# Kernel tuning notes

Hardware: AMD Instinct MI355X
Metric: run time of the kernel (lower is better)

The kernel has to match this reference:

```python
import jax, jax.numpy as jnp
import numpy as np

B, T = 4096, 2048
ETA = 10.0  # constant['eta']


def setup_inputs() -> dict:
    key = jax.random.key(0)
    k0, k1, k2 = jax.random.split(key, 3)
    return {
        "inputs": jax.random.normal(k0, (B, T, 2), dtype=jnp.float32),  # [:,:,0]=eps, [:,:,1]=hs (step size)
        "W1": jax.random.normal(k1, (2, 16), dtype=jnp.float32) * 0.5,
        "b1": jnp.zeros((16,), dtype=jnp.float32),
        "W2": jax.random.normal(k2, (16, 1), dtype=jnp.float32) * 0.5,
        "b2": jnp.zeros((1,), dtype=jnp.float32),
    }


def reference(inputs, W1, b1, W2, b2):
    # GSM recurrent cell: e = MLP([eps, gamma]); sig = de/deps; gamma' = gamma - hs/eta * de/dgamma.
    # Analytic gradient of scalar e w.r.t. x (softplus' = sigmoid):
    #   de/dx = (sigmoid(x @ W1 + b1) * W2[:, 0]) @ W1.T      # [B, 2]
    inv_eta = 1.0 / ETA
    w2 = W2[:, 0]  # [16]

    def step(gamma, inp_t):  # gamma: [B,1], inp_t: [B,2]
        eps = inp_t[:, 0:1]
        hs = inp_t[:, 1:2]
        x = jnp.concatenate([eps, gamma], axis=1)            # [B,2]
        z1 = x @ W1 + b1                                     # [B,16]
        de_dx = (jax.nn.sigmoid(z1) * w2) @ W1.T             # [B,2]
        sig = de_dx[:, 0:1]                                  # de/deps
        gamma_n = gamma - hs * inv_eta * de_dx[:, 1:2]       # de/dgamma update
        return gamma_n, sig

    gamma0 = jnp.zeros((inputs.shape[0], 1), dtype=inputs.dtype)
    _, sig_seq = jax.lax.scan(step, gamma0, jnp.swapaxes(inputs, 0, 1))  # sig_seq: [T,B,1]
    return jnp.swapaxes(sig_seq, 0, 1)  # [B,T,1]
```

## Files before the change

kernel.cpp:

```cpp
#include <hip/hip_runtime.h>

#define B_ROWS 4096
#define T_LEN  2048
#define TB     16
#define NBLK   (T_LEN / TB)

template<int CTRL>
__device__ __forceinline__ float dpp_add(float x) {
  int y = __builtin_amdgcn_update_dpp(0, __builtin_bit_cast(int, x),
                                      CTRL, 0xf, 0xf, true);
  return x + __builtin_bit_cast(float, y);
}

__device__ __forceinline__ float allreduce16(float x) {
  x = dpp_add<0xB1>(x);
  x = dpp_add<0x4E>(x);
  x = dpp_add<0x141>(x);
  x = dpp_add<0x140>(x);
  return x;
}

struct Blk { float4 q[8]; };

__device__ __forceinline__ void load_blk(const float4* __restrict__ src,
                                         Blk& b) {
#pragma unroll
  for (int i = 0; i < 8; ++i) b.q[i] = src[i];
}

__device__ __forceinline__ void compute_blk(const Blk& b, float& gamma,
                                            float w0n, float w1n, float bnn,
                                            float c0, float c1, int j,
                                            float* __restrict__ outp) {
  float pre[TB], hs[TB];
#pragma unroll
  for (int i = 0; i < 8; ++i) {
    pre[2 * i]     = fmaf(b.q[i].x, w0n, bnn);
    hs[2 * i]      = b.q[i].y;
    pre[2 * i + 1] = fmaf(b.q[i].z, w0n, bnn);
    hs[2 * i + 1]  = b.q[i].w;
  }
  float keep = 0.0f;
#pragma unroll
  for (int t = 0; t < TB; ++t) {
    float z  = fmaf(gamma, w1n, pre[t]);
    float e  = __builtin_amdgcn_exp2f(z);
    float r  = __builtin_amdgcn_rcpf(1.0f + e);
    float s1 = allreduce16(r * c1);
    gamma    = fmaf(-hs[t], s1, gamma);
    float s0 = allreduce16(r * c0);
    keep     = (j == t) ? s0 : keep;
  }
  outp[j] = keep;
}

__global__ __launch_bounds__(64) void gsm_scan_kernel(
    const float* __restrict__ inp, const float* __restrict__ W1f,
    const float* __restrict__ b1f, const float* __restrict__ W2f,
    float* __restrict__ out) {
  const int lane = threadIdx.x;
  const int grp  = lane >> 4;
  const int j    = lane & 15;
  const int row  = (blockIdx.x << 2) + grp;

  const float LOG2E = 1.4426950408889634f;
  const float w0n = -LOG2E * W1f[j];
  const float w1n = -LOG2E * W1f[16 + j];
  const float bnn = -LOG2E * b1f[j];
  const float w2j = W2f[j];
  const float c0  = w2j * W1f[j];
  const float c1  = w2j * W1f[16 + j] * 0.1f;

  const float4* src = (const float4*)(inp + (size_t)row * (2 * T_LEN));
  float* outrow = out + (size_t)row * T_LEN;

  float gamma = 0.0f;
  Blk A, Bb;
  load_blk(src, A);

#pragma unroll 1
  for (int b = 0; b < NBLK; b += 2) {
    load_blk(src + (size_t)(b + 1) * 8, Bb);
    compute_blk(A, gamma, w0n, w1n, bnn, c0, c1, j, outrow + b * TB);
    if (b + 2 < NBLK) load_blk(src + (size_t)(b + 2) * 8, A);
    compute_blk(Bb, gamma, w0n, w1n, bnn, c0, c1, j, outrow + (b + 1) * TB);
  }
}

extern "C" void kernel_launch(void* const* d_in, const int* in_sizes, int n_in,
                              void* d_out, int out_size, void* d_ws,
                              size_t ws_size, hipStream_t stream) {
  const float* inp = (const float*)d_in[0];
  const float* W1  = (const float*)d_in[1];
  const float* b1  = (const float*)d_in[2];
  const float* W2  = (const float*)d_in[3];
  float* out = (float*)d_out;

  dim3 grid(B_ROWS / 4);
  dim3 block(64);
  hipLaunchKernelGGL(gsm_scan_kernel, grid, block, 0, stream,
                     inp, W1, b1, W2, out);
}
```

Before: 146.4 us.

## Split each row across two 16-lane halves for gamma and sigma reductions

Each row is now handled by 32 lanes instead of 16. One half computes the gamma-gradient reduction and the other computes the sigma reduction, so each timestep runs one allreduce instead of two serialized ones. The updated gamma is broadcast from the low half via a DPP row broadcast. The per-lane weight is folded into the denominator via 1/c to save a multiply. The grid doubles and each wave covers two rows instead of four, halving per-wave throughput while shortening the dependent chain. Dividing by c risks inf or NaN if any w2*W1 product is zero.

```diff
diff --git a/kernel.cpp b/kernel.cpp
--- a/kernel.cpp
+++ b/kernel.cpp
@@ -20,6 +20,12 @@
   return x;
 }
 
+__device__ __forceinline__ float bcast_low16(float g) {
+  int gi = __builtin_bit_cast(int, g);
+  int y  = __builtin_amdgcn_update_dpp(gi, gi, 0x142, 0xA, 0xF, false);
+  return __builtin_bit_cast(float, y);
+}
+
 struct Blk { float4 q[8]; };
 
 __device__ __forceinline__ void load_blk(const float4* __restrict__ src,
@@ -30,28 +36,29 @@
 
 __device__ __forceinline__ void compute_blk(const Blk& b, float& gamma,
                                             float w0n, float w1n, float bnn,
-                                            float c0, float c1, int j,
+                                            float invc, int j, bool out_half,
                                             float* __restrict__ outp) {
-  float pre[TB], hs[TB];
+  float pre[TB], hsn[TB];
 #pragma unroll
   for (int i = 0; i < 8; ++i) {
     pre[2 * i]     = fmaf(b.q[i].x, w0n, bnn);
-    hs[2 * i]      = b.q[i].y;
+    hsn[2 * i]     = -b.q[i].y;
     pre[2 * i + 1] = fmaf(b.q[i].z, w0n, bnn);
-    hs[2 * i + 1]  = b.q[i].w;
+    hsn[2 * i + 1] = -b.q[i].w;
   }
   float keep = 0.0f;
 #pragma unroll
   for (int t = 0; t < TB; ++t) {
-    float z  = fmaf(gamma, w1n, pre[t]);
-    float e  = __builtin_amdgcn_exp2f(z);
-    float r  = __builtin_amdgcn_rcpf(1.0f + e);
-    float s1 = allreduce16(r * c1);
-    gamma    = fmaf(-hs[t], s1, gamma);
-    float s0 = allreduce16(r * c0);
-    keep     = (j == t) ? s0 : keep;
+    float z = fmaf(gamma, w1n, pre[t]);
+    float e = __builtin_amdgcn_exp2f(z);
+    float d = fmaf(e, invc, invc);
+    float v = __builtin_amdgcn_rcpf(d);
+    float s = allreduce16(v);
+    gamma   = fmaf(hsn[t], s, gamma);
+    gamma   = bcast_low16(gamma);
+    keep    = (j == t) ? s : keep;
   }
-  outp[j] = keep;
+  if (out_half) outp[j] = keep;
 }
 
 __global__ __launch_bounds__(64) void gsm_scan_kernel(
@@ -59,20 +66,23 @@
     const float* __restrict__ b1f, const float* __restrict__ W2f,
     float* __restrict__ out) {
   const int lane = threadIdx.x;
-  const int grp  = lane >> 4;
+  const int rid  = lane >> 5;
+  const int half = (lane >> 4) & 1;
   const int j    = lane & 15;
-  const int row  = (blockIdx.x << 2) + grp;
+  const int row  = (blockIdx.x << 1) + rid;
 
   const float LOG2E = 1.4426950408889634f;
   const float w0n = -LOG2E * W1f[j];
   const float w1n = -LOG2E * W1f[16 + j];
   const float bnn = -LOG2E * b1f[j];
   const float w2j = W2f[j];
-  const float c0  = w2j * W1f[j];
-  const float c1  = w2j * W1f[16 + j] * 0.1f;
+  const float c   = half ? (w2j * W1f[j])
+                         : (w2j * W1f[16 + j] * 0.1f);
+  const float invc = 1.0f / c;
 
   const float4* src = (const float4*)(inp + (size_t)row * (2 * T_LEN));
   float* outrow = out + (size_t)row * T_LEN;
+  const bool out_half = (half == 1);
 
   float gamma = 0.0f;
   Blk A, Bb;
@@ -81,9 +91,10 @@
 #pragma unroll 1
   for (int b = 0; b < NBLK; b += 2) {
     load_blk(src + (size_t)(b + 1) * 8, Bb);
-    compute_blk(A, gamma, w0n, w1n, bnn, c0, c1, j, outrow + b * TB);
+    compute_blk(A, gamma, w0n, w1n, bnn, invc, j, out_half, outrow + b * TB);
     if (b + 2 < NBLK) load_blk(src + (size_t)(b + 2) * 8, A);
-    compute_blk(Bb, gamma, w0n, w1n, bnn, c0, c1, j, outrow + (b + 1) * TB);
+    compute_blk(Bb, gamma, w0n, w1n, bnn, invc, j, out_half,
+                outrow + (b + 1) * TB);
   }
 }
 
@@ -96,7 +107,7 @@
   const float* W2  = (const float*)d_in[3];
   float* out = (float*)d_out;
 
-  dim3 grid(B_ROWS / 4);
+  dim3 grid(B_ROWS / 2);
   dim3 block(64);
   hipLaunchKernelGGL(gsm_scan_kernel, grid, block, 0, stream,
                      inp, W1, b1, W2, out);
```

Measured after the change: 137.2 us. 1.07x faster.

## Carry pre-activation z across steps and fold c1 into sigmoid reciprocal

Applied to the files above, without the earlier changes.

The recurrence now carries the pre-activation z instead of gamma: each step adds a precomputed difference of input projections and subtracts hs*w1n times the reduced sum. The c1 scale is folded into the sigmoid denominator, so r*c1 comes straight from one rcp, and the s0 term becomes r*ratio, which shortens the serial dependency chain between the exp and the next step. Block loading is reorganised so each block is extracted into a precomputed struct before its compute, and the first input of the next block is peeked to bridge the boundary. The trade-off is possible numerical differences when c1 is near zero (inf/NaN from 1/c1) and more registers held live.

```diff
diff --git a/kernel.cpp b/kernel.cpp
--- a/kernel.cpp
+++ b/kernel.cpp
@@ -28,28 +28,42 @@
   for (int i = 0; i < 8; ++i) b.q[i] = src[i];
 }
 
-__device__ __forceinline__ void compute_blk(const Blk& b, float& gamma,
-                                            float w0n, float w1n, float bnn,
-                                            float c0, float c1, int j,
-                                            float* __restrict__ outp) {
-  float pre[TB], hs[TB];
+struct Pre { float dpre[TB - 1]; float hw[TB]; float pre15; };
+
+__device__ __forceinline__ void extract(const Blk& b, float w0n, float bnn,
+                                        float w1n, Pre& p) {
+  float pre[TB];
 #pragma unroll
   for (int i = 0; i < 8; ++i) {
-    pre[2 * i]     = fmaf(b.q[i].x, w0n, bnn);
-    hs[2 * i]      = b.q[i].y;
-    pre[2 * i + 1] = fmaf(b.q[i].z, w0n, bnn);
-    hs[2 * i + 1]  = b.q[i].w;
+    pre[2 * i]       = fmaf(b.q[i].x, w0n, bnn);
+    p.hw[2 * i]      = b.q[i].y * w1n;
+    pre[2 * i + 1]   = fmaf(b.q[i].z, w0n, bnn);
+    p.hw[2 * i + 1]  = b.q[i].w * w1n;
   }
+#pragma unroll
+  for (int t = 0; t < TB - 1; ++t) p.dpre[t] = pre[t + 1] - pre[t];
+  p.pre15 = pre[TB - 1];
+}
+
+__device__ __forceinline__ void compute16(const Pre& p, float nextq0x,
+                                          bool peek, float& z, float invc1,
+                                          float ratio, float w0n, float bnn,
+                                          int j, float* __restrict__ outp) {
   float keep = 0.0f;
 #pragma unroll
   for (int t = 0; t < TB; ++t) {
-    float z  = fmaf(gamma, w1n, pre[t]);
     float e  = __builtin_amdgcn_exp2f(z);
-    float r  = __builtin_amdgcn_rcpf(1.0f + e);
-    float s1 = allreduce16(r * c1);
-    gamma    = fmaf(-hs[t], s1, gamma);
-    float s0 = allreduce16(r * c0);
-    keep     = (j == t) ? s0 : keep;
+    float d  = fmaf(e, invc1, invc1);
+    float r  = __builtin_amdgcn_rcpf(d);
+    float s1 = allreduce16(r);
+    float dpre_t = (t < TB - 1)
+                     ? p.dpre[t]
+                     : (peek ? (fmaf(nextq0x, w0n, bnn) - p.pre15) : 0.0f);
+    float P  = z + dpre_t;
+    float v0 = r * ratio;
+    float s0 = allreduce16(v0);
+    z    = fmaf(-p.hw[t], s1, P);
+    keep = (j == t) ? s0 : keep;
   }
   outp[j] = keep;
 }
@@ -70,20 +84,28 @@
   const float w2j = W2f[j];
   const float c0  = w2j * W1f[j];
   const float c1  = w2j * W1f[16 + j] * 0.1f;
+  const float invc1 = 1.0f / c1;
+  const float ratio = c0 * invc1;
 
   const float4* src = (const float4*)(inp + (size_t)row * (2 * T_LEN));
   float* outrow = out + (size_t)row * T_LEN;
 
-  float gamma = 0.0f;
   Blk A, Bb;
+  Pre p;
   load_blk(src, A);
+  load_blk(src + 8, Bb);
+  float z = fmaf(A.q[0].x, w0n, bnn);
 
 #pragma unroll 1
   for (int b = 0; b < NBLK; b += 2) {
-    load_blk(src + (size_t)(b + 1) * 8, Bb);
-    compute_blk(A, gamma, w0n, w1n, bnn, c0, c1, j, outrow + b * TB);
+    extract(A, w0n, bnn, w1n, p);
     if (b + 2 < NBLK) load_blk(src + (size_t)(b + 2) * 8, A);
-    compute_blk(Bb, gamma, w0n, w1n, bnn, c0, c1, j, outrow + (b + 1) * TB);
+    compute16(p, Bb.q[0].x, true, z, invc1, ratio, w0n, bnn, j,
+              outrow + b * TB);
+    extract(Bb, w0n, bnn, w1n, p);
+    if (b + 3 < NBLK) load_blk(src + (size_t)(b + 3) * 8, Bb);
+    compute16(p, A.q[0].x, (b + 2 < NBLK), z, invc1, ratio, w0n, bnn, j,
+              outrow + (b + 1) * TB);
   }
 }
 
```

Measured after the change: 119.6 us. 1.22x faster.

## Split hidden units four per lane and carry pre-activations incrementally

Applied to the files above, without the earlier changes.

Each lane now handles four hidden units instead of one, so a row needs a 4-lane quad rather than 16 lanes. The two 16-lane DPP reductions per step shrink to 2-step quad reductions, and each wave covers 16 rows instead of 4. The pre-activation z is updated incrementally from the eps delta and the gamma update. The c1 scaling is folded into the reciprocal denominator and c0 is expressed as a ratio to c1. This shortens the serial dependency chain per timestep and cuts the number of blocks, at the cost of more per-lane arithmetic, fewer waves, and possible precision drift from the incremental z (and division by zero if a W2*W1 product is zero).

```diff
diff --git a/kernel.cpp b/kernel.cpp
--- a/kernel.cpp
+++ b/kernel.cpp
@@ -7,16 +7,13 @@
 
 template<int CTRL>
 __device__ __forceinline__ float dpp_add(float x) {
-  int y = __builtin_amdgcn_update_dpp(0, __builtin_bit_cast(int, x),
-                                      CTRL, 0xf, 0xf, true);
+  int y = __builtin_amdgcn_mov_dpp(__builtin_bit_cast(int, x),
+                                   CTRL, 0xf, 0xf, true);
   return x + __builtin_bit_cast(float, y);
 }
-
-__device__ __forceinline__ float allreduce16(float x) {
+__device__ __forceinline__ float quad_allreduce(float x) {
   x = dpp_add<0xB1>(x);
   x = dpp_add<0x4E>(x);
-  x = dpp_add<0x141>(x);
-  x = dpp_add<0x140>(x);
   return x;
 }
 
@@ -28,30 +25,45 @@
   for (int i = 0; i < 8; ++i) b.q[i] = src[i];
 }
 
-__device__ __forceinline__ void compute_blk(const Blk& b, float& gamma,
-                                            float w0n, float w1n, float bnn,
-                                            float c0, float c1, int j,
-                                            float* __restrict__ outp) {
-  float pre[TB], hs[TB];
-#pragma unroll
-  for (int i = 0; i < 8; ++i) {
-    pre[2 * i]     = fmaf(b.q[i].x, w0n, bnn);
-    hs[2 * i]      = b.q[i].y;
-    pre[2 * i + 1] = fmaf(b.q[i].z, w0n, bnn);
-    hs[2 * i + 1]  = b.q[i].w;
-  }
-  float keep = 0.0f;
+__device__ __forceinline__ void compute16(
+    const Blk& bk, float nextq0x, bool peek, float4& z,
+    const float4 w0n, const float4 w1n, const float4 invc1,
+    const float4 ratio, int q, float* __restrict__ outp) {
+  float4 kp = make_float4(0.f, 0.f, 0.f, 0.f);
 #pragma unroll
   for (int t = 0; t < TB; ++t) {
-    float z  = fmaf(gamma, w1n, pre[t]);
-    float e  = __builtin_amdgcn_exp2f(z);
-    float r  = __builtin_amdgcn_rcpf(1.0f + e);
-    float s1 = allreduce16(r * c1);
-    gamma    = fmaf(-hs[t], s1, gamma);
-    float s0 = allreduce16(r * c0);
-    keep     = (j == t) ? s0 : keep;
+    const float eps  = (t & 1) ? bk.q[t >> 1].z : bk.q[t >> 1].x;
+    const float hs   = (t & 1) ? bk.q[t >> 1].w : bk.q[t >> 1].y;
+    const float epsn = (t == TB - 1) ? (peek ? nextq0x : eps)
+                       : ((t & 1) ? bk.q[(t + 1) >> 1].x : bk.q[t >> 1].z);
+    float e0 = __builtin_amdgcn_exp2f(z.x);
+    float e1 = __builtin_amdgcn_exp2f(z.y);
+    float e2 = __builtin_amdgcn_exp2f(z.z);
+    float e3 = __builtin_amdgcn_exp2f(z.w);
+    float r0 = __builtin_amdgcn_rcpf(fmaf(e0, invc1.x, invc1.x));
+    float r1 = __builtin_amdgcn_rcpf(fmaf(e1, invc1.y, invc1.y));
+    float r2 = __builtin_amdgcn_rcpf(fmaf(e2, invc1.z, invc1.z));
+    float r3 = __builtin_amdgcn_rcpf(fmaf(e3, invc1.w, invc1.w));
+    float s1 = quad_allreduce((r0 + r1) + (r2 + r3));
+    float deps = epsn - eps;
+    float P0 = fmaf(deps, w0n.x, z.x);
+    float P1 = fmaf(deps, w0n.y, z.y);
+    float P2 = fmaf(deps, w0n.z, z.z);
+    float P3 = fmaf(deps, w0n.w, z.w);
+    float hn = -hs;
+    z.x = fmaf(hn * w1n.x, s1, P0);
+    z.y = fmaf(hn * w1n.y, s1, P1);
+    z.z = fmaf(hn * w1n.z, s1, P2);
+    z.w = fmaf(hn * w1n.w, s1, P3);
+    float s0 = quad_allreduce(fmaf(r0, ratio.x, r1 * ratio.y) +
+                              fmaf(r2, ratio.z, r3 * ratio.w));
+    const bool mine = ((t >> 2) == q);
+    if ((t & 3) == 0) kp.x = mine ? s0 : kp.x;
+    if ((t & 3) == 1) kp.y = mine ? s0 : kp.y;
+    if ((t & 3) == 2) kp.z = mine ? s0 : kp.z;
+    if ((t & 3) == 3) kp.w = mine ? s0 : kp.w;
   }
-  outp[j] = keep;
+  *(float4*)(outp + 4 * q) = kp;
 }
 
 __global__ __launch_bounds__(64) void gsm_scan_kernel(
@@ -59,31 +71,55 @@
     const float* __restrict__ b1f, const float* __restrict__ W2f,
     float* __restrict__ out) {
   const int lane = threadIdx.x;
-  const int grp  = lane >> 4;
-  const int j    = lane & 15;
-  const int row  = (blockIdx.x << 2) + grp;
+  const int q    = lane & 3;
+  const int row  = (blockIdx.x << 4) + (lane >> 2);
+  const int u0   = q << 2;
 
   const float LOG2E = 1.4426950408889634f;
-  const float w0n = -LOG2E * W1f[j];
-  const float w1n = -LOG2E * W1f[16 + j];
-  const float bnn = -LOG2E * b1f[j];
-  const float w2j = W2f[j];
-  const float c0  = w2j * W1f[j];
-  const float c1  = w2j * W1f[16 + j] * 0.1f;
+  const float4 W0 = *(const float4*)&W1f[u0];
+  const float4 Wr = *(const float4*)&W1f[16 + u0];
+  const float4 B1 = *(const float4*)&b1f[u0];
+  const float4 W2 = *(const float4*)&W2f[u0];
+
+  float4 w0n, w1n, bnn, invc1, ratio;
+  w0n.x = -LOG2E * W0.x; w0n.y = -LOG2E * W0.y;
+  w0n.z = -LOG2E * W0.z; w0n.w = -LOG2E * W0.w;
+  w1n.x = -LOG2E * Wr.x; w1n.y = -LOG2E * Wr.y;
+  w1n.z = -LOG2E * Wr.z; w1n.w = -LOG2E * Wr.w;
+  bnn.x = -LOG2E * B1.x; bnn.y = -LOG2E * B1.y;
+  bnn.z = -LOG2E * B1.z; bnn.w = -LOG2E * B1.w;
+  invc1.x = 1.0f / (0.1f * W2.x * Wr.x);  ratio.x = (W2.x * W0.x) * invc1.x * 0.0f + (W2.x * W0.x) * (0.1f * W2.x * Wr.x == 0.f ? 0.f : 1.0f / (0.1f * W2.x * Wr.x));
+  invc1.x = 1.0f / (0.1f * W2.x * Wr.x);
+  invc1.y = 1.0f / (0.1f * W2.y * Wr.y);
+  invc1.z = 1.0f / (0.1f * W2.z * Wr.z);
+  invc1.w = 1.0f / (0.1f * W2.w * Wr.w);
+  ratio.x = (W2.x * W0.x) * invc1.x;
+  ratio.y = (W2.y * W0.y) * invc1.y;
+  ratio.z = (W2.z * W0.z) * invc1.z;
+  ratio.w = (W2.w * W0.w) * invc1.w;
 
   const float4* src = (const float4*)(inp + (size_t)row * (2 * T_LEN));
   float* outrow = out + (size_t)row * T_LEN;
 
-  float gamma = 0.0f;
   Blk A, Bb;
   load_blk(src, A);
+  load_blk(src + 8, Bb);
+  float4 z;
+  z.x = fmaf(A.q[0].x, w0n.x, bnn.x);
+  z.y = fmaf(A.q[0].x, w0n.y, bnn.y);
+  z.z = fmaf(A.q[0].x, w0n.z, bnn.z);
+  z.w = fmaf(A.q[0].x, w0n.w, bnn.w);
 
 #pragma unroll 1
   for (int b = 0; b < NBLK; b += 2) {
-    load_blk(src + (size_t)(b + 1) * 8, Bb);
-    compute_blk(A, gamma, w0n, w1n, bnn, c0, c1, j, outrow + b * TB);
+    Blk cur = A;
     if (b + 2 < NBLK) load_blk(src + (size_t)(b + 2) * 8, A);
-    compute_blk(Bb, gamma, w0n, w1n, bnn, c0, c1, j, outrow + (b + 1) * TB);
+    compute16(cur, Bb.q[0].x, true, z, w0n, w1n, invc1, ratio, q,
+              outrow + b * TB);
+    Blk cur2 = Bb;
+    if (b + 3 < NBLK) load_blk(src + (size_t)(b + 3) * 8, Bb);
+    compute16(cur2, A.q[0].x, (b + 2 < NBLK), z, w0n, w1n, invc1, ratio, q,
+              outrow + (b + 1) * TB);
   }
 }
 
@@ -96,7 +132,7 @@
   const float* W2  = (const float*)d_in[3];
   float* out = (float*)d_out;
 
-  dim3 grid(B_ROWS / 4);
+  dim3 grid(B_ROWS / 16);
   dim3 block(64);
   hipLaunchKernelGGL(gsm_scan_kernel, grid, block, 0, stream,
                      inp, W1, b1, W2, out);
```

Result: slower. 199.2 us (+36.1%).
